# Kernel optimization log

Hardware: AMD Instinct MI355X
Metric: run time of the kernel (lower is better)

Reference implementation:

```python
import jax, jax.numpy as jnp
import numpy as np

TEMPERATURE = 0.001
EPS = 1e-12  # torch F.normalize eps


def _l2_normalize(x):
    norm = jnp.sqrt(jnp.sum(x * x, axis=1, keepdims=True))
    return x / jnp.maximum(norm, EPS)


def setup_inputs() -> dict:
    key = jax.random.key(0)
    k1, k2 = jax.random.split(key)
    B, D = 4096, 256
    proj_1 = jax.random.normal(k1, (B, D), dtype=jnp.float32)
    proj_2 = jax.random.normal(k2, (B, D), dtype=jnp.float32)
    return {"proj_1": proj_1, "proj_2": proj_2}


def reference(proj_1, proj_2):
    B = proj_1.shape[0]
    z_i = _l2_normalize(proj_1)  # [B, D]
    z_j = _l2_normalize(proj_2)  # [B, D]
    reps = jnp.concatenate([z_i, z_j], axis=0)  # [2B, D]
    # cosine similarity of unit vectors == dot product -> one GEMM instead of
    # the broadcast (2B,2B,D) tensor the torch code implicitly materializes
    sim = reps @ reps.T  # [2B, 2B]
    # diag(sim, +B) and diag(sim, -B) are both <z_i[k], z_j[k]>
    pos = jnp.sum(z_i * z_j, axis=1)  # [B]
    positives = jnp.concatenate([pos, pos], axis=0)  # [2B]
    logits = sim / TEMPERATURE  # [2B, 2B]
    # NOTE: original code logsumexps over the FULL row (diagonal included);
    # the masked `denominator` it computes is never used. Replicate faithfully.
    lse = jax.nn.logsumexp(logits, axis=1)  # [2B]
    all_losses = -(positives / TEMPERATURE) + lse
    loss = jnp.sum(all_losses) / (2 * B)
    return (loss, jnp.sum(positives))
```

## Files before the change

### kernel.cpp

```cpp
#include <hip/hip_runtime.h>
#include <hip/hip_bf16.h>

#define B_ROWS 4096
#define D_DIM  256
#define TWO_B  8192

typedef float f32x4  __attribute__((ext_vector_type(4)));
typedef short bf16x8 __attribute__((ext_vector_type(8)));

#define CCHUNK      512
#define TPS         2
#define STAGE_BYTES (TPS * 8192)
#define NSTAGES     (CCHUNK / (TPS * 16))
#define MT          4
#define GY          (TWO_B / CCHUNK)

#define SC2 1442.6951f
#define M0  1442.6951f

#define WAITVM(N) do { asm volatile("s_waitcnt vmcnt(" #N ")" ::: "memory"); \
                       __builtin_amdgcn_sched_barrier(0); } while (0)

__device__ __forceinline__ void async_copy16(void* lds_dst, const void* gsrc) {
    __builtin_amdgcn_global_load_lds(
        (__attribute__((address_space(1))) void*)(gsrc),
        (__attribute__((address_space(3))) void*)(lds_dst), 16, 0, 0);
}

__global__ __launch_bounds__(256) void k_prep(const float* __restrict__ p1,
                                              const float* __restrict__ p2,
                                              __hip_bfloat16* __restrict__ reps,
                                              float* __restrict__ pos) {
    const int r = blockIdx.x;
    const int t = threadIdx.x;
    float e1 = p1[r * D_DIM + t];
    float e2 = p2[r * D_DIM + t];
    float s11 = e1 * e1, s22 = e2 * e2, s12 = e1 * e2;
    #pragma unroll
    for (int m = 1; m < 64; m <<= 1) {
        s11 += __shfl_xor(s11, m);
        s22 += __shfl_xor(s22, m);
        s12 += __shfl_xor(s12, m);
    }
    __shared__ float red[3][4];
    const int w = t >> 6, l = t & 63;
    if (l == 0) { red[0][w] = s11; red[1][w] = s22; red[2][w] = s12; }
    __syncthreads();
    s11 = red[0][0] + red[0][1] + red[0][2] + red[0][3];
    s22 = red[1][0] + red[1][1] + red[1][2] + red[1][3];
    s12 = red[2][0] + red[2][1] + red[2][2] + red[2][3];
    const float n1 = fmaxf(sqrtf(s11), 1e-12f);
    const float n2 = fmaxf(sqrtf(s22), 1e-12f);
    reps[r * D_DIM + t]            = __float2bfloat16(e1 / n1);
    reps[(B_ROWS + r) * D_DIM + t] = __float2bfloat16(e2 / n2);
    if (t == 0) pos[r] = s12 / (n1 * n2);
}

__global__ __launch_bounds__(256, 2) void k_simlse(const __hip_bfloat16* __restrict__ reps,
                                                   float* __restrict__ s_part) {
    __shared__ char lds[3][STAGE_BYTES];
    const int t   = threadIdx.x;
    const int w   = t >> 6;
    const int l   = t & 63;
    const int c16 = l & 15;
    const int g   = l >> 4;

    const int row_base = blockIdx.x * 256 + w * 64;
    const int gy       = blockIdx.y;
    const int col_base = gy * CCHUNK;
    const char* repsB = (const char*)reps;

    bf16x8 afrag[MT][8];
    #pragma unroll
    for (int mt = 0; mt < MT; ++mt) {
        const int arow = row_base + mt * 16 + c16;
        #pragma unroll
        for (int kk = 0; kk < 8; ++kk)
            afrag[mt][kk] = *(const bf16x8*)(repsB + (size_t)arow * 512 + kk * 64 + g * 16);
    }

    float s[4 * MT];
    #pragma unroll
    for (int i = 0; i < 4 * MT; ++i) s[i] = 0.f;

    auto stage = [&](char* buf, int cstage) {
        #pragma unroll
        for (int i = 0; i < STAGE_BYTES / 4096; ++i) {
            const int a  = i * 4096 + w * 1024 + l * 16;
            const int tt = a >> 13;
            const int rr = a & 8191;
            const int kk = rr >> 10;
            const int gg = (rr >> 8) & 3;
            const int cc = (rr >> 4) & 15;
            const int col = cstage + tt * 16 + cc;
            async_copy16(buf + i * 4096 + w * 1024,
                         repsB + (size_t)col * 512 + kk * 64 + gg * 16);
        }
    };

    auto compute = [&](const char* buf) {
        #pragma unroll
        for (int tt = 0; tt < TPS; ++tt) {
            f32x4 acc[MT];
            #pragma unroll
            for (int mt = 0; mt < MT; ++mt) acc[mt] = f32x4{0.f, 0.f, 0.f, 0.f};
            #pragma unroll
            for (int kk = 0; kk < 8; ++kk) {
                const bf16x8 b = *(const bf16x8*)(buf + tt * 8192 + kk * 1024 + l * 16);
                #pragma unroll
                for (int mt = 0; mt < MT; ++mt)
                    acc[mt] = __builtin_amdgcn_mfma_f32_16x16x32_bf16(afrag[mt][kk], b, acc[mt], 0, 0, 0);
            }
            float tmax = acc[0][0];
            #pragma unroll
            for (int mt = 0; mt < MT; ++mt)
                #pragma unroll
                for (int r = 0; r < 4; ++r) tmax = fmaxf(tmax, acc[mt][r]);
            if (__any(tmax > 0.90f)) {
                #pragma unroll
                for (int mt = 0; mt < MT; ++mt)
                    #pragma unroll
                    for (int r = 0; r < 4; ++r)
                        s[mt * 4 + r] += exp2f(acc[mt][r] * SC2 - M0);
            }
        }
    };

    stage(lds[0], col_base);
    stage(lds[1], col_base + TPS * 16);

    char* bA = lds[0];
    char* bB = lds[1];
    char* bC = lds[2];
    for (int st = 0; st < NSTAGES; ++st) {
        if (st + 2 < NSTAGES) {
            WAITVM(4);
            __builtin_amdgcn_s_barrier();
            stage(bC, col_base + (st + 2) * (TPS * 16));
        } else if (st + 2 == NSTAGES) {
            WAITVM(4);
            __builtin_amdgcn_s_barrier();
        } else {
            WAITVM(0);
            __builtin_amdgcn_s_barrier();
        }
        compute(bA);
        char* tmp = bA; bA = bB; bB = bC; bC = tmp;
    }

    #pragma unroll
    for (int i = 0; i < 4 * MT; ++i) {
        #pragma unroll
        for (int m = 1; m < 16; m <<= 1) s[i] += __shfl_xor(s[i], m);
    }
    if (c16 == 0) {
        #pragma unroll
        for (int mt = 0; mt < MT; ++mt)
            #pragma unroll
            for (int r = 0; r < 4; ++r)
                s_part[(size_t)(row_base + mt * 16 + g * 4 + r) * GY + gy] = s[mt * 4 + r];
    }
}

__global__ __launch_bounds__(256) void k_red(const float* __restrict__ s_part,
                                             const float* __restrict__ pos,
                                             float* __restrict__ red_buf) {
    const float LN2 = 0.69314718f;
    const int wg = blockIdx.x;
    const int t  = threadIdx.x;
    const int r  = wg * 256 + t;
    const f32x4* p4 = (const f32x4*)(s_part + (size_t)r * GY);
    float srow = 0.f;
    #pragma unroll
    for (int i = 0; i < GY / 4; ++i) {
        const f32x4 a = p4[i];
        srow += (a[0] + a[1]) + (a[2] + a[3]);
    }
    float lsum = LN2 * (M0 + log2f(srow)) - 1000.0f * pos[r & (B_ROWS - 1)];
    float psum = (t < 128) ? pos[wg * 128 + t] : 0.f;
    #pragma unroll
    for (int m = 1; m < 64; m <<= 1) {
        lsum += __shfl_xor(lsum, m);
        psum += __shfl_xor(psum, m);
    }
    __shared__ float red[2][4];
    const int w = t >> 6, l = t & 63;
    if (l == 0) { red[0][w] = lsum; red[1][w] = psum; }
    __syncthreads();
    if (t == 0) {
        red_buf[wg]      = red[0][0] + red[0][1] + red[0][2] + red[0][3];
        red_buf[32 + wg] = red[1][0] + red[1][1] + red[1][2] + red[1][3];
    }
}

__global__ __launch_bounds__(64) void k_final2(const float* __restrict__ red_buf,
                                               float* __restrict__ out) {
    const int t = threadIdx.x;
    float v = (t < 32) ? red_buf[t] : red_buf[32 + (t - 32)];
    #pragma unroll
    for (int m = 1; m < 32; m <<= 1) v += __shfl_xor(v, m);
    if (t == 0)  out[0] = v / (float)TWO_B;
    if (t == 32) out[1] = 2.0f * v;
}

extern "C" void kernel_launch(void* const* d_in, const int* in_sizes, int n_in,
                              void* d_out, int out_size, void* d_ws, size_t ws_size,
                              hipStream_t stream) {
    const float* p1 = (const float*)d_in[0];
    const float* p2 = (const float*)d_in[1];
    float* out = (float*)d_out;
    char* ws = (char*)d_ws;

    __hip_bfloat16* reps = (__hip_bfloat16*)ws;
    float* pos     = (float*)(ws + (size_t)TWO_B * D_DIM * 2);
    float* s_part  = (float*)(ws + (size_t)TWO_B * D_DIM * 2 + B_ROWS * 4);
    float* red_buf = s_part + (size_t)TWO_B * GY;

    k_prep<<<B_ROWS, 256, 0, stream>>>(p1, p2, reps, pos);
    dim3 g2(TWO_B / 256, GY);
    k_simlse<<<g2, 256, 0, stream>>>(reps, s_part);
    k_red<<<32, 256, 0, stream>>>(s_part, pos, red_buf);
    k_final2<<<1, 64, 0, stream>>>(red_buf, out);
}
```

Measured before the change: 53.47 us.

## Use single-wave blocks with private double-buffered LDS to drop barriers

Turns the similarity/LSE kernel into 64-thread single-wavefront workgroups. Each one streams its own 16-column B tiles through a two-slot LDS double buffer, so workgroup barriers are no longer needed and only the wave's own vmcnt/lgkmcnt waits remain. The cost it targets is s_barrier stalls and the cross-wave coupling of the shared 3-stage pipeline. In exchange, B tiles are no longer shared by four waves, so global/L2 traffic for the column data rises roughly fourfold and there are more, smaller workgroups. Prefetch depth also drops to one stage ahead.

```diff
diff --git a/kernel.cpp b/kernel.cpp
--- a/kernel.cpp
+++ b/kernel.cpp
@@ -8,18 +8,18 @@
 typedef float f32x4  __attribute__((ext_vector_type(4)));
 typedef short bf16x8 __attribute__((ext_vector_type(8)));
 
-#define CCHUNK      512
-#define TPS         2
-#define STAGE_BYTES (TPS * 8192)
-#define NSTAGES     (CCHUNK / (TPS * 16))
-#define MT          4
-#define GY          (TWO_B / CCHUNK)
+#define CCHUNK  512
+#define NST     (CCHUNK / 16)
+#define MT      4
+#define GY      (TWO_B / CCHUNK)
 
 #define SC2 1442.6951f
 #define M0  1442.6951f
 
 #define WAITVM(N) do { asm volatile("s_waitcnt vmcnt(" #N ")" ::: "memory"); \
                        __builtin_amdgcn_sched_barrier(0); } while (0)
+#define DRAIN_LDS() do { asm volatile("s_waitcnt lgkmcnt(0)" ::: "memory"); \
+                         __builtin_amdgcn_sched_barrier(0); } while (0)
 
 __device__ __forceinline__ void async_copy16(void* lds_dst, const void* gsrc) {
     __builtin_amdgcn_global_load_lds(
@@ -56,16 +56,14 @@
     if (t == 0) pos[r] = s12 / (n1 * n2);
 }
 
-__global__ __launch_bounds__(256, 2) void k_simlse(const __hip_bfloat16* __restrict__ reps,
-                                                   float* __restrict__ s_part) {
-    __shared__ char lds[3][STAGE_BYTES];
-    const int t   = threadIdx.x;
-    const int w   = t >> 6;
-    const int l   = t & 63;
+__global__ __launch_bounds__(64, 2) void k_simlse(const __hip_bfloat16* __restrict__ reps,
+                                                  float* __restrict__ s_part) {
+    __shared__ char lds[2][8192];
+    const int l   = threadIdx.x;
     const int c16 = l & 15;
     const int g   = l >> 4;
 
-    const int row_base = blockIdx.x * 256 + w * 64;
+    const int row_base = blockIdx.x * 64;
     const int gy       = blockIdx.y;
     const int col_base = gy * CCHUNK;
     const char* repsB = (const char*)reps;
@@ -85,67 +83,56 @@
 
     auto stage = [&](char* buf, int cstage) {
         #pragma unroll
-        for (int i = 0; i < STAGE_BYTES / 4096; ++i) {
-            const int a  = i * 4096 + w * 1024 + l * 16;
-            const int tt = a >> 13;
-            const int rr = a & 8191;
-            const int kk = rr >> 10;
-            const int gg = (rr >> 8) & 3;
-            const int cc = (rr >> 4) & 15;
-            const int col = cstage + tt * 16 + cc;
-            async_copy16(buf + i * 4096 + w * 1024,
+        for (int i = 0; i < 8; ++i) {
+            const int a  = i * 1024 + l * 16;
+            const int kk = a >> 10;
+            const int gg = (a >> 8) & 3;
+            const int cc = (a >> 4) & 15;
+            const int col = cstage + cc;
+            async_copy16(buf + i * 1024,
                          repsB + (size_t)col * 512 + kk * 64 + gg * 16);
         }
     };
 
     auto compute = [&](const char* buf) {
-        #pragma unroll
-        for (int tt = 0; tt < TPS; ++tt) {
-            f32x4 acc[MT];
-            #pragma unroll
-            for (int mt = 0; mt < MT; ++mt) acc[mt] = f32x4{0.f, 0.f, 0.f, 0.f};
-            #pragma unroll
-            for (int kk = 0; kk < 8; ++kk) {
-                const bf16x8 b = *(const bf16x8*)(buf + tt * 8192 + kk * 1024 + l * 16);
-                #pragma unroll
-                for (int mt = 0; mt < MT; ++mt)
-                    acc[mt] = __builtin_amdgcn_mfma_f32_16x16x32_bf16(afrag[mt][kk], b, acc[mt], 0, 0, 0);
-            }
-            float tmax = acc[0][0];
+        f32x4 acc[MT];
+        #pragma unroll
+        for (int mt = 0; mt < MT; ++mt) acc[mt] = f32x4{0.f, 0.f, 0.f, 0.f};
+        #pragma unroll
+        for (int kk = 0; kk < 8; ++kk) {
+            const bf16x8 b = *(const bf16x8*)(buf + kk * 1024 + l * 16);
+            #pragma unroll
+            for (int mt = 0; mt < MT; ++mt)
+                acc[mt] = __builtin_amdgcn_mfma_f32_16x16x32_bf16(afrag[mt][kk], b, acc[mt], 0, 0, 0);
+        }
+        float tmax = acc[0][0];
+        #pragma unroll
+        for (int mt = 0; mt < MT; ++mt)
+            #pragma unroll
+            for (int r = 0; r < 4; ++r) tmax = fmaxf(tmax, acc[mt][r]);
+        if (__any(tmax > 0.90f)) {
             #pragma unroll
             for (int mt = 0; mt < MT; ++mt)
                 #pragma unroll
-                for (int r = 0; r < 4; ++r) tmax = fmaxf(tmax, acc[mt][r]);
-            if (__any(tmax > 0.90f)) {
-                #pragma unroll
-                for (int mt = 0; mt < MT; ++mt)
-                    #pragma unroll
-                    for (int r = 0; r < 4; ++r)
-                        s[mt * 4 + r] += exp2f(acc[mt][r] * SC2 - M0);
-            }
+                for (int r = 0; r < 4; ++r)
+                    s[mt * 4 + r] += exp2f(acc[mt][r] * SC2 - M0);
         }
     };
 
     stage(lds[0], col_base);
-    stage(lds[1], col_base + TPS * 16);
-
-    char* bA = lds[0];
-    char* bB = lds[1];
-    char* bC = lds[2];
-    for (int st = 0; st < NSTAGES; ++st) {
-        if (st + 2 < NSTAGES) {
-            WAITVM(4);
-            __builtin_amdgcn_s_barrier();
-            stage(bC, col_base + (st + 2) * (TPS * 16));
-        } else if (st + 2 == NSTAGES) {
-            WAITVM(4);
-            __builtin_amdgcn_s_barrier();
+    stage(lds[1], col_base + 16);
+
+    for (int st = 0; st < NST; ++st) {
+        if (st + 1 < NST) {
+            WAITVM(8);
         } else {
             WAITVM(0);
-            __builtin_amdgcn_s_barrier();
-        }
-        compute(bA);
-        char* tmp = bA; bA = bB; bB = bC; bC = tmp;
+        }
+        compute(lds[st & 1]);
+        if (st + 2 < NST) {
+            DRAIN_LDS();
+            stage(lds[st & 1], col_base + (st + 2) * 16);
+        }
     }
 
     #pragma unroll
@@ -217,8 +204,8 @@
     float* red_buf = s_part + (size_t)TWO_B * GY;
 
     k_prep<<<B_ROWS, 256, 0, stream>>>(p1, p2, reps, pos);
-    dim3 g2(TWO_B / 256, GY);
-    k_simlse<<<g2, 256, 0, stream>>>(reps, s_part);
+    dim3 g2(TWO_B / 64, GY);
+    k_simlse<<<g2, 64, 0, stream>>>(reps, s_part);
     k_red<<<32, 256, 0, stream>>>(s_part, pos, red_buf);
     k_final2<<<1, 64, 0, stream>>>(red_buf, out);
 }
```

Result: slower. 82.93 us (+55.1%).
